# Optimization experiments

Hardware: AMD Instinct MI355X
Metric: run time of the kernel (lower is better)

The kernel has to match this reference:

```python
import jax, jax.numpy as jnp
import numpy as np

TOPK = 1024
C = 32
FC0 = 256
EPS_BN = 1e-5
EPS_NORM = 1e-12


def setup_inputs() -> dict:
    key = jax.random.key(0)
    ks = jax.random.split(key, 8)
    B, L = 128, 16384
    N = B * L
    x = jax.random.normal(ks[0], (N, C), dtype=jnp.float32)
    length = jnp.full((B,), L, dtype=jnp.int32)
    # conv1d_1: Conv1d(32, 1, 1) -> weight [1, 32, 1] ~ vector [32], bias [1]
    w_att = jax.random.normal(ks[1], (C,), dtype=jnp.float32) * (1.0 / np.sqrt(C))
    b_att = jnp.zeros((1,), dtype=jnp.float32)
    # bn_1: BatchNorm1d(1) (eval mode: use running stats)
    g1 = jnp.ones((1,), dtype=jnp.float32)
    be1 = jnp.zeros((1,), dtype=jnp.float32)
    rm1 = jnp.zeros((1,), dtype=jnp.float32)
    rv1 = jnp.ones((1,), dtype=jnp.float32)
    # fc_1: Linear(TOPK*C, FC0)
    fan_in = TOPK * C
    W_fc = jax.random.normal(ks[2], (FC0, fan_in), dtype=jnp.float32) * (1.0 / np.sqrt(fan_in))
    b_fc = jnp.zeros((FC0,), dtype=jnp.float32)
    # bn_2: BatchNorm1d(FC0) (eval mode)
    g2 = jnp.ones((FC0,), dtype=jnp.float32)
    be2 = jnp.zeros((FC0,), dtype=jnp.float32)
    rm2 = jnp.zeros((FC0,), dtype=jnp.float32)
    rv2 = jnp.ones((FC0,), dtype=jnp.float32)
    return {"x": x, "length": length, "w_att": w_att, "b_att": b_att,
            "g1": g1, "be1": be1, "rm1": rm1, "rv1": rv1,
            "W_fc": W_fc, "b_fc": b_fc,
            "g2": g2, "be2": be2, "rm2": rm2, "rv2": rv2}


def reference(x, length, w_att, b_att, g1, be1, rm1, rv1, W_fc, b_fc, g2, be2, rm2, rv2):
    B = length.shape[0]
    N = x.shape[0]
    L = N // B  # equal-length segments (sum(length) == N)
    # attention score: 1x1 conv over channels + BatchNorm1d(1) (eval)
    att = x @ w_att + b_att[0]                                   # [N]
    att = (att - rm1[0]) * (g1[0] / jnp.sqrt(rv1[0] + EPS_BN)) + be1[0]
    # per-segment descending sort + take top TOPK == top_k per segment
    att_b = att.reshape(B, L)                                    # [B, L]
    x_b = x.reshape(B, L, C)                                     # [B, L, C]
    _, idx = jax.lax.top_k(att_b, TOPK)                          # [B, TOPK]
    ranked = jnp.take_along_axis(x_b, idx[:, :, None], axis=1)   # [B, TOPK, C]
    flat = ranked.reshape(B, TOPK * C)                           # [B, TOPK*C]
    # fc_1 + bn_2 (eval) + L2 row-normalize
    out = flat @ W_fc.T + b_fc                                   # [B, FC0]
    out = (out - rm2) * (g2 / jnp.sqrt(rv2 + EPS_BN)) + be2
    nrm = jnp.maximum(jnp.linalg.norm(out, axis=1, keepdims=True), EPS_NORM)
    return out / nrm
```

## Files before the change

### kernel.cpp

```cpp
#include <hip/hip_runtime.h>
#include <stdint.h>

#define CC 32
#define TOPK 1024
#define FC0 256

__global__ __launch_bounds__(256)
void k_att(const float* __restrict__ x,
           const float* __restrict__ w_att, const float* __restrict__ b_att,
           uint32_t* __restrict__ key, int N)
{
    __shared__ float tile[256][CC + 1];
    const int t = threadIdx.x;
    const size_t base = (size_t)blockIdx.x * 256;
    const float4* xv = (const float4*)(x + base * CC);
    #pragma unroll
    for (int i = 0; i < 8; ++i) {
        int e = i * 256 + t;
        float4 v = xv[e];
        int r = e >> 3, c4 = (e & 7) * 4;
        tile[r][c4 + 0] = v.x; tile[r][c4 + 1] = v.y;
        tile[r][c4 + 2] = v.z; tile[r][c4 + 3] = v.w;
    }
    __syncthreads();
    float p[8];
    #pragma unroll
    for (int j = 0; j < 8; ++j) {
        float pj = __fmul_rn(tile[t][j], w_att[j]);
        pj = __fmaf_rn(tile[t][8 + j],  w_att[8 + j],  pj);
        pj = __fmaf_rn(tile[t][16 + j], w_att[16 + j], pj);
        pj = __fmaf_rn(tile[t][24 + j], w_att[24 + j], pj);
        p[j] = pj;
    }
    float q0 = __fadd_rn(p[0], p[1]);
    float q1 = __fadd_rn(p[2], p[3]);
    float q2 = __fadd_rn(p[4], p[5]);
    float q3 = __fadd_rn(p[6], p[7]);
    float dot = __fadd_rn(__fadd_rn(q0, q1), __fadd_rn(q2, q3));
    float v = __fadd_rn(dot, b_att[0]);
    uint32_t bits = __float_as_uint(v);
    key[base + t] = (bits & 0x80000000u) ? ~bits : (bits | 0x80000000u);
}

__device__ __forceinline__ uint64_t cex(uint64_t v, int s, bool up, int t)
{
    uint64_t o = (uint64_t)__shfl_xor((unsigned long long)v, s, 64);
    bool left = ((t & s) == 0);
    uint64_t mn = v < o ? v : o;
    uint64_t mx = v < o ? o : v;
    return (left == up) ? mn : mx;
}

__global__ __launch_bounds__(1024)
void k_topk(const uint32_t* __restrict__ key, int* __restrict__ idx_out, int L)
{
    __shared__ uint32_t kv[16384];
    __shared__ uint64_t cv[2048];
    __shared__ uint32_t hist[257];
    __shared__ uint32_t s_prefix, s_k, s_cnt;
    const int t = threadIdx.x;
    const int b = blockIdx.x;
    const int lane = t & 63;
    const uint32_t* kseg = key + (size_t)b * L;
    for (int i = t; i < L; i += 1024) kv[i] = kseg[i];
    if (t == 0) { s_prefix = 0; s_k = TOPK; s_cnt = 0; }
    __syncthreads();
    #pragma unroll
    for (int round = 0; round < 2; ++round) {
        if (t < 257) hist[t] = 0;
        __syncthreads();
        const uint32_t pref = s_prefix;
        const uint32_t k = s_k;
        for (int i = t; i < L; i += 1024) {
            uint32_t u = kv[i];
            if (round == 0) atomicAdd(&hist[u >> 24], 1u);
            else if ((u >> 24) == pref) atomicAdd(&hist[(u >> 16) & 255u], 1u);
        }
        __syncthreads();
        if (t < 64) {
            int l = t;
            uint32_t h0 = hist[4*l], h1 = hist[4*l+1], h2 = hist[4*l+2], h3 = hist[4*l+3];
            uint32_t s3 = h3, s2 = h2 + s3, s1 = h1 + s2, s0 = h0 + s1;
            uint32_t tot = s0, run = tot;
            #pragma unroll
            for (int off = 1; off < 64; off <<= 1) {
                int src = l + off < 64 ? l + off : 63;
                uint32_t o = __shfl(run, src, 64);
                if (l + off < 64) run += o;
            }
            uint32_t esuf = run - tot;
            hist[4*l]   = s0 + esuf; hist[4*l+1] = s1 + esuf;
            hist[4*l+2] = s2 + esuf; hist[4*l+3] = s3 + esuf;
        }
        __syncthreads();
        if (t < 256) {
            uint32_t st = hist[t], sn = hist[t + 1];
            if (st >= k && sn < k) {
                s_prefix = (pref << 8) | (uint32_t)t;
                s_k = k - sn;
            }
        }
        __syncthreads();
    }
    const uint32_t T = s_prefix << 16;
    for (int i = t; i < L; i += 1024) {
        bool q = kv[i] >= T;
        unsigned long long m = __ballot(q);
        uint32_t base = 0;
        if (lane == 0 && m)
            base = atomicAdd(&s_cnt, (uint32_t)__popcll(m));
        base = __shfl(base, 0);
        if (q) {
            uint32_t pos = base + (uint32_t)__popcll(m & ((1ULL << lane) - 1ULL));
            if (pos < 2048)
                cv[pos] = ((uint64_t)kv[i] << 32) | (uint64_t)(uint32_t)(~(uint32_t)i);
        }
    }
    __syncthreads();
    const uint32_t mm = s_cnt < 2048u ? s_cnt : 2048u;
    for (int i = t; i < 2048; i += 1024)
        if ((uint32_t)i >= mm) cv[i] = 0ULL;
    __syncthreads();
    {
        uint64_t r0 = cv[t], r1 = cv[t + 1024];
        #pragma unroll
        for (int size = 2; size <= 64; size <<= 1) {
            bool up = ((t & size) == 0);
            #pragma unroll
            for (int s = size >> 1; s > 0; s >>= 1) {
                r0 = cex(r0, s, up, t);
                r1 = cex(r1, s, up, t);
            }
        }
        cv[t] = r0; cv[t + 1024] = r1;
    }
    #pragma unroll
    for (int size = 128; size <= 2048; size <<= 1) {
        for (int s = size >> 1; s >= 64; s >>= 1) {
            __syncthreads();
            int i = ((t & ~(s - 1)) << 1) | (t & (s - 1));
            int j = i | s;
            uint64_t va = cv[i], vb = cv[j];
            bool up = ((i & size) == 0);
            if (up ? (va > vb) : (va < vb)) { cv[i] = vb; cv[j] = va; }
        }
        __syncthreads();
        {
            uint64_t a0 = cv[t], a1 = cv[t + 1024];
            bool up0, up1;
            if (size <= 512)      { up0 = ((t & size) == 0); up1 = up0; }
            else if (size == 1024){ up0 = true;  up1 = false; }
            else                  { up0 = true;  up1 = true;  }
            #pragma unroll
            for (int s = 32; s > 0; s >>= 1) {
                a0 = cex(a0, s, up0, t);
                a1 = cex(a1, s, up1, t);
            }
            cv[t] = a0; cv[t + 1024] = a1;
        }
        __syncthreads();
    }
    if (t < TOPK)
        idx_out[(size_t)b * TOPK + t] = (int)(~(uint32_t)cv[2047 - t]);
}

#define FT 64
#define KCI 32
#define NKC 128
#define KCHUNK 256

__global__ __launch_bounds__(256)
void k_fc(const float* __restrict__ x, const int* __restrict__ idx,
          const float* __restrict__ W, float* __restrict__ part, int L)
{
    __shared__ float flT[KCI][128];
    __shared__ float wT[KCI][FT];
    const int t = threadIdx.x;
    const int kc = blockIdx.x;
    const int fb = blockIdx.y * FT;
    const int tb = t >> 4, tf = t & 15;
    float acc[8][4];
    #pragma unroll
    for (int i = 0; i < 8; ++i)
        #pragma unroll
        for (int j = 0; j < 4; ++j) acc[i][j] = 0.f;

    const int b_ld = t >> 1, half = t & 1;
    for (int sub = 0; sub < KCHUNK / KCI; ++sub) {
        const int kbase = kc * KCHUNK + sub * KCI;
        const int t_idx = kbase >> 5;
        {
            int row = idx[b_ld * TOPK + t_idx];
            row = row < 0 ? 0 : (row >= L ? L - 1 : row);
            const float* src = x + ((size_t)b_ld * L + row) * CC + half * 16;
            #pragma unroll
            for (int q = 0; q < 4; ++q) {
                float4 v = ((const float4*)src)[q];
                int c0 = half * 16 + q * 4;
                flT[c0 + 0][b_ld] = v.x; flT[c0 + 1][b_ld] = v.y;
                flT[c0 + 2][b_ld] = v.z; flT[c0 + 3][b_ld] = v.w;
            }
        }
        {
            int idx512 = t + 256 * 0;
            #pragma unroll
            for (int i2 = 0; i2 < 2; ++i2) {
                int e = t + i2 * 256;
                int fl = e >> 3, u = e & 7;
                const float4 v = *(const float4*)(W + (size_t)(fb + fl) * (TOPK * CC) + kbase + u * 4);
                wT[u * 4 + 0][fl] = v.x; wT[u * 4 + 1][fl] = v.y;
                wT[u * 4 + 2][fl] = v.z; wT[u * 4 + 3][fl] = v.w;
            }
            (void)idx512;
        }
        __syncthreads();
        #pragma unroll
        for (int kk = 0; kk < KCI; ++kk) {
            float bb[8], ww[4];
            *(float4*)&bb[0] = *(const float4*)&flT[kk][tb * 8];
            *(float4*)&bb[4] = *(const float4*)&flT[kk][tb * 8 + 4];
            *(float4*)&ww[0] = *(const float4*)&wT[kk][tf * 4];
            #pragma unroll
            for (int i = 0; i < 8; ++i)
                #pragma unroll
                for (int j = 0; j < 4; ++j)
                    acc[i][j] = fmaf(bb[i], ww[j], acc[i][j]);
        }
        __syncthreads();
    }
    float* pbase = part + ((size_t)kc * 128) * 256 + fb + tf * 4;
    #pragma unroll
    for (int i = 0; i < 8; ++i) {
        float* dst = pbase + (size_t)(tb * 8 + i) * 256;
        ((float4*)dst)[0] = make_float4(acc[i][0], acc[i][1], acc[i][2], acc[i][3]);
    }
}

__global__ __launch_bounds__(256)
void k_post(const float* __restrict__ part, const float* __restrict__ b_fc,
            const float* __restrict__ g2, const float* __restrict__ be2,
            const float* __restrict__ rm2, const float* __restrict__ rv2,
            float* __restrict__ out)
{
    __shared__ float red[256];
    const int b = blockIdx.x, f = threadIdx.x;
    float s = 0.f;
    #pragma unroll 8
    for (int kc = 0; kc < NKC; ++kc)
        s += part[((size_t)kc * 128 + b) * 256 + f];
    s += b_fc[f];
    float o = (s - rm2[f]) * (g2[f] / sqrtf(rv2[f] + 1e-5f)) + be2[f];
    red[f] = o * o;
    __syncthreads();
    for (int st = 128; st > 0; st >>= 1) {
        if (f < st) red[f] += red[f + st];
        __syncthreads();
    }
    float nrm = fmaxf(sqrtf(red[0]), 1e-12f);
    out[(size_t)b * 256 + f] = o / nrm;
}

extern "C" void kernel_launch(void* const* d_in, const int* in_sizes, int n_in,
                              void* d_out, int out_size, void* d_ws, size_t ws_size,
                              hipStream_t stream)
{
    const float* x     = (const float*)d_in[0];
    const float* w_att = (const float*)d_in[2];
    const float* b_att = (const float*)d_in[3];
    const float* W_fc  = (const float*)d_in[8];
    const float* b_fc  = (const float*)d_in[9];
    const float* g2    = (const float*)d_in[10];
    const float* be2   = (const float*)d_in[11];
    const float* rm2   = (const float*)d_in[12];
    const float* rv2   = (const float*)d_in[13];

    const int N = in_sizes[0] / CC;
    const int B = in_sizes[1];
    const int L = N / B;

    uint8_t* ws = (uint8_t*)d_ws;
    uint32_t* key = (uint32_t*)(ws);
    int* idx      = (int*)(ws + (size_t)N * 4);
    float* part   = (float*)(ws + (size_t)N * 4 + (size_t)B * TOPK * 4);

    k_att<<<N / 256, 256, 0, stream>>>(x, w_att, b_att, key, N);
    k_topk<<<B, 1024, 0, stream>>>(key, idx, L);
    dim3 g3(NKC, FC0 / FT);
    k_fc<<<g3, 256, 0, stream>>>(x, idx, W_fc, part, L);
    k_post<<<B, 256, 0, stream>>>(part, b_fc, g2, be2, rm2, rv2, (float*)d_out);
}
```

Measured before the change: 116.9 us.

## Fuse attention scoring into top-k and split segments into halves with bitonic merge

```diff
diff --git a/kernel.cpp b/kernel.cpp
--- a/kernel.cpp
+++ b/kernel.cpp
@@ -4,43 +4,7 @@
 #define CC 32
 #define TOPK 1024
 #define FC0 256
-
-__global__ __launch_bounds__(256)
-void k_att(const float* __restrict__ x,
-           const float* __restrict__ w_att, const float* __restrict__ b_att,
-           uint32_t* __restrict__ key, int N)
-{
-    __shared__ float tile[256][CC + 1];
-    const int t = threadIdx.x;
-    const size_t base = (size_t)blockIdx.x * 256;
-    const float4* xv = (const float4*)(x + base * CC);
-    #pragma unroll
-    for (int i = 0; i < 8; ++i) {
-        int e = i * 256 + t;
-        float4 v = xv[e];
-        int r = e >> 3, c4 = (e & 7) * 4;
-        tile[r][c4 + 0] = v.x; tile[r][c4 + 1] = v.y;
-        tile[r][c4 + 2] = v.z; tile[r][c4 + 3] = v.w;
-    }
-    __syncthreads();
-    float p[8];
-    #pragma unroll
-    for (int j = 0; j < 8; ++j) {
-        float pj = __fmul_rn(tile[t][j], w_att[j]);
-        pj = __fmaf_rn(tile[t][8 + j],  w_att[8 + j],  pj);
-        pj = __fmaf_rn(tile[t][16 + j], w_att[16 + j], pj);
-        pj = __fmaf_rn(tile[t][24 + j], w_att[24 + j], pj);
-        p[j] = pj;
-    }
-    float q0 = __fadd_rn(p[0], p[1]);
-    float q1 = __fadd_rn(p[2], p[3]);
-    float q2 = __fadd_rn(p[4], p[5]);
-    float q3 = __fadd_rn(p[6], p[7]);
-    float dot = __fadd_rn(__fadd_rn(q0, q1), __fadd_rn(q2, q3));
-    float v = __fadd_rn(dot, b_att[0]);
-    uint32_t bits = __float_as_uint(v);
-    key[base + t] = (bits & 0x80000000u) ? ~bits : (bits | 0x80000000u);
-}
+#define HL 8192
 
 __device__ __forceinline__ uint64_t cex(uint64_t v, int s, bool up, int t)
 {
@@ -52,26 +16,64 @@
 }
 
 __global__ __launch_bounds__(1024)
-void k_topk(const uint32_t* __restrict__ key, int* __restrict__ idx_out, int L)
-{
-    __shared__ uint32_t kv[16384];
+void k_seltop(const float* __restrict__ x,
+              const float* __restrict__ w_att, const float* __restrict__ b_att,
+              uint64_t* __restrict__ cand)
+{
+    __shared__ float tile[512][CC + 1];
+    __shared__ uint32_t kv[HL];
     __shared__ uint64_t cv[2048];
     __shared__ uint32_t hist[257];
     __shared__ uint32_t s_prefix, s_k, s_cnt;
     const int t = threadIdx.x;
     const int b = blockIdx.x;
     const int lane = t & 63;
-    const uint32_t* kseg = key + (size_t)b * L;
-    for (int i = t; i < L; i += 1024) kv[i] = kseg[i];
+    const uint32_t halfbase = (uint32_t)(b & 1) * HL;
+
     if (t == 0) { s_prefix = 0; s_k = TOPK; s_cnt = 0; }
-    __syncthreads();
+
+    for (int c = 0; c < 16; ++c) {
+        const size_t rowbase = (size_t)b * HL + (size_t)c * 512;
+        const float4* xv = (const float4*)(x + rowbase * CC);
+        __syncthreads();
+        #pragma unroll
+        for (int i = 0; i < 4; ++i) {
+            int e = i * 1024 + t;
+            float4 v = xv[e];
+            int r = e >> 3, c4 = (e & 7) * 4;
+            tile[r][c4 + 0] = v.x; tile[r][c4 + 1] = v.y;
+            tile[r][c4 + 2] = v.z; tile[r][c4 + 3] = v.w;
+        }
+        __syncthreads();
+        if (t < 512) {
+            float p[8];
+            #pragma unroll
+            for (int j = 0; j < 8; ++j) {
+                float pj = __fmul_rn(tile[t][j], w_att[j]);
+                pj = __fmaf_rn(tile[t][8 + j],  w_att[8 + j],  pj);
+                pj = __fmaf_rn(tile[t][16 + j], w_att[16 + j], pj);
+                pj = __fmaf_rn(tile[t][24 + j], w_att[24 + j], pj);
+                p[j] = pj;
+            }
+            float q0 = __fadd_rn(p[0], p[1]);
+            float q1 = __fadd_rn(p[2], p[3]);
+            float q2 = __fadd_rn(p[4], p[5]);
+            float q3 = __fadd_rn(p[6], p[7]);
+            float dot = __fadd_rn(__fadd_rn(q0, q1), __fadd_rn(q2, q3));
+            float v = __fadd_rn(dot, b_att[0]);
+            uint32_t bits = __float_as_uint(v);
+            kv[c * 512 + t] = (bits & 0x80000000u) ? ~bits : (bits | 0x80000000u);
+        }
+    }
+    __syncthreads();
+
     #pragma unroll
     for (int round = 0; round < 2; ++round) {
         if (t < 257) hist[t] = 0;
         __syncthreads();
         const uint32_t pref = s_prefix;
         const uint32_t k = s_k;
-        for (int i = t; i < L; i += 1024) {
+        for (int i = t; i < HL; i += 1024) {
             uint32_t u = kv[i];
             if (round == 0) atomicAdd(&hist[u >> 24], 1u);
             else if ((u >> 24) == pref) atomicAdd(&hist[(u >> 16) & 255u], 1u);
@@ -103,7 +105,8 @@
         __syncthreads();
     }
     const uint32_t T = s_prefix << 16;
-    for (int i = t; i < L; i += 1024) {
+
+    for (int i = t; i < HL; i += 1024) {
         bool q = kv[i] >= T;
         unsigned long long m = __ballot(q);
         uint32_t base = 0;
@@ -113,7 +116,8 @@
         if (q) {
             uint32_t pos = base + (uint32_t)__popcll(m & ((1ULL << lane) - 1ULL));
             if (pos < 2048)
-                cv[pos] = ((uint64_t)kv[i] << 32) | (uint64_t)(uint32_t)(~(uint32_t)i);
+                cv[pos] = ((uint64_t)kv[i] << 32)
+                        | (uint64_t)(uint32_t)(~(halfbase + (uint32_t)i));
         }
     }
     __syncthreads();
@@ -121,6 +125,7 @@
     for (int i = t; i < 2048; i += 1024)
         if ((uint32_t)i >= mm) cv[i] = 0ULL;
     __syncthreads();
+
     {
         uint64_t r0 = cv[t], r1 = cv[t + 1024];
         #pragma unroll
@@ -160,8 +165,26 @@
         }
         __syncthreads();
     }
-    if (t < TOPK)
-        idx_out[(size_t)b * TOPK + t] = (int)(~(uint32_t)cv[2047 - t]);
+    cand[(size_t)b * TOPK + t] = cv[2047 - t];
+}
+
+__global__ __launch_bounds__(1024)
+void k_merge(const uint64_t* __restrict__ cand, int* __restrict__ idx_out)
+{
+    __shared__ uint64_t cv[2048];
+    const int t = threadIdx.x;
+    const int seg = blockIdx.x;
+    cv[t]        = cand[(size_t)(seg * 2) * TOPK + t];
+    cv[1024 + t] = cand[(size_t)(seg * 2 + 1) * TOPK + (1023 - t)];
+    __syncthreads();
+    for (int s = 1024; s >= 1; s >>= 1) {
+        int i = ((t & ~(s - 1)) << 1) | (t & (s - 1));
+        int j = i | s;
+        uint64_t va = cv[i], vb = cv[j];
+        if (va < vb) { cv[i] = vb; cv[j] = va; }
+        __syncthreads();
+    }
+    idx_out[(size_t)seg * TOPK + t] = (int)(~(uint32_t)cv[t]);
 }
 
 #define FT 64
@@ -202,7 +225,6 @@
             }
         }
         {
-            int idx512 = t + 256 * 0;
             #pragma unroll
             for (int i2 = 0; i2 < 2; ++i2) {
                 int e = t + i2 * 256;
@@ -211,7 +233,6 @@
                 wT[u * 4 + 0][fl] = v.x; wT[u * 4 + 1][fl] = v.y;
                 wT[u * 4 + 2][fl] = v.z; wT[u * 4 + 3][fl] = v.w;
             }
-            (void)idx512;
         }
         __syncthreads();
         #pragma unroll
@@ -279,12 +300,12 @@
     const int L = N / B;
 
     uint8_t* ws = (uint8_t*)d_ws;
-    uint32_t* key = (uint32_t*)(ws);
-    int* idx      = (int*)(ws + (size_t)N * 4);
-    float* part   = (float*)(ws + (size_t)N * 4 + (size_t)B * TOPK * 4);
-
-    k_att<<<N / 256, 256, 0, stream>>>(x, w_att, b_att, key, N);
-    k_topk<<<B, 1024, 0, stream>>>(key, idx, L);
+    uint64_t* cand = (uint64_t*)(ws);
+    int* idx       = (int*)(ws + (size_t)2 * B * TOPK * 8);
+    float* part    = (float*)(ws + (size_t)2 * B * TOPK * 8 + (size_t)B * TOPK * 4);
+
+    k_seltop<<<2 * B, 1024, 0, stream>>>(x, w_att, b_att, cand);
+    k_merge<<<B, 1024, 0, stream>>>(cand, idx);
     dim3 g3(NKC, FC0 / FT);
     k_fc<<<g3, 256, 0, stream>>>(x, idx, W_fc, part, L);
     k_post<<<B, 256, 0, stream>>>(part, b_fc, g2, be2, rm2, rv2, (float*)d_out);
```

Measured after the change: 115.4 us. No clear change (-1.3%).
